# Kernel optimization log

Hardware: AMD Instinct MI355X
Metric: run time of the kernel (lower is better)

Reference implementation:

```python
import jax, jax.numpy as jnp
import numpy as np

B, D, N, M = 32, 512, 1024, 1024

def setup_inputs() -> dict:
    key = jax.random.key(0)
    k1, k2 = jax.random.split(key)
    embedding_1 = jax.random.normal(k1, (B, D, N), dtype=jnp.float32)
    embedding_2 = jax.random.normal(k2, (B, D, M), dtype=jnp.float32)
    return {"embedding_1": embedding_1, "embedding_2": embedding_2}

def reference(embedding_1, embedding_2):
    # att[b, n, m] = sum_d e1[b, d, n] * e2[b, d, m]   (bmm of e1^T with e2)
    att = jnp.einsum('bdn,bdm->bnm', embedding_1, embedding_2)
    # double max-pool: max over m then over n -> global max of score matrix
    s = jnp.max(att, axis=(-1, -2))  # [B]
    return s[:, None]  # [B, 1]
```

## Files before the change

### kernel.cpp

```cpp
#include <hip/hip_runtime.h>
#include <hip/hip_bf16.h>

#define B_ 32
#define D_ 512
#define N_ 1024
#define M_ 1024
#define BT 256
#define BK 64
#define NIT 16

typedef __attribute__((ext_vector_type(8))) short bf16x8;
typedef __attribute__((ext_vector_type(4))) short s16x4;
typedef __attribute__((ext_vector_type(4))) float f32x4;
typedef __attribute__((ext_vector_type(4))) int   i32x4;
typedef unsigned short ushort_t;

__device__ __forceinline__ unsigned map_f(float f) {
    unsigned b = __float_as_uint(f);
    return (b & 0x80000000u) ? ~b : (b | 0x80000000u);
}

struct __align__(16) GSmem {
    ushort_t As[2][BT * BK];
    ushort_t Bs[2][BT * BK];
    float red[8];
};

__device__ __forceinline__ void load_tile(const float* __restrict__ p, int k0,
                                          int krb, int gr, float4* fl) {
    #pragma unroll
    for (int it = 0; it < 4; ++it) {
        const float* q = p + (size_t)(k0 + krb + it) * N_ + gr * 8;
        fl[2 * it]     = *reinterpret_cast<const float4*>(q);
        fl[2 * it + 1] = *reinterpret_cast<const float4*>(q + 4);
    }
}

__device__ __forceinline__ void flush_tile(char* lds, int krb, int gr, const float4* fl) {
    #pragma unroll
    for (int it = 0; it < 4; ++it) {
        const int k = krb + it;
        const float4& f0 = fl[2 * it];
        const float4& f1 = fl[2 * it + 1];
        __hip_bfloat162 h0 = __float22bfloat162_rn(make_float2(f0.x, f0.y));
        __hip_bfloat162 h1 = __float22bfloat162_rn(make_float2(f0.z, f0.w));
        __hip_bfloat162 h2 = __float22bfloat162_rn(make_float2(f1.x, f1.y));
        __hip_bfloat162 h3 = __float22bfloat162_rn(make_float2(f1.z, f1.w));
        i32x4 v = { *reinterpret_cast<const int*>(&h0), *reinterpret_cast<const int*>(&h1),
                    *reinterpret_cast<const int*>(&h2), *reinterpret_cast<const int*>(&h3) };
        *reinterpret_cast<i32x4*>(lds + k * 512 + 16 * (gr ^ (2 * (k & 3)))) = v;
    }
}

__global__ __launch_bounds__(512, 2)
void fused_gemm_max_kernel(const float* __restrict__ e1, const float* __restrict__ e2,
                           float* __restrict__ out) {
    __shared__ GSmem sm;
    const int wg  = blockIdx.x;
    const int swz = (wg & 7) * 32 + (wg >> 3);
    const int b    = swz >> 3;
    const int pair = swz & 7;
    const int tn  = (pair >> 1) * BT;
    const int tc0 = (pair & 1) * 512;

    const int t    = threadIdx.x;
    const int lane = t & 63;
    const int wave = t >> 6;
    const int wrow = (wave >> 2) * 128;
    const int wcol = (wave & 3) * 64;

    const int krb = (t >> 5) * 4;
    const int gr  = t & 31;

    const int c = lane & 15, g = lane >> 4;
    const int r = c >> 2, d = (c >> 1) & 1, h = c & 1;

    unsigned tbA[8], tbB[4];
    #pragma unroll
    for (int m = 0; m < 8; ++m)
        tbA[m] = (unsigned)((8 * g + r) * 512
               + 16 * ((((wrow >> 3) + 2 * m + d) ^ (2 * r))) + 8 * h);
    #pragma unroll
    for (int n = 0; n < 4; ++n)
        tbB[n] = (unsigned)(65536 + (8 * g + r) * 512
               + 16 * ((((wcol >> 3) + 2 * n + d) ^ (2 * r))) + 8 * h);
    const unsigned ldsbase = (unsigned)(uintptr_t)&sm.As[0][0];

    const float* Ap  = e1 + (size_t)b * D_ * N_ + tn;
    const float* Bp0 = e2 + (size_t)b * D_ * M_ + tc0;
    const float* Bp1 = Bp0 + BT;

    f32x4 acc[8][4] = {};
    float4 fl[8];
    float tmax = -3.4e38f;

    load_tile(Ap, 0, krb, gr, fl);
    flush_tile((char*)sm.As[0], krb, gr, fl);
    load_tile(Bp0, 0, krb, gr, fl);
    flush_tile((char*)sm.Bs[0], krb, gr, fl);
    load_tile(Ap, BK, krb, gr, fl);
    asm volatile("s_waitcnt lgkmcnt(0)" ::: "memory");
    __builtin_amdgcn_s_barrier();

    int cur = 0;
    #pragma unroll 1
    for (int it = 0; it < NIT; ++it) {
        const unsigned off = ldsbase + (unsigned)cur * 32768u;
        const bool has_next = (it < NIT - 1);

        #pragma unroll
        for (int kk = 0; kk < 2; ++kk) {
            s16x4 alo[8], ahi[8], blo[4], bhi[4];
            #pragma unroll
            for (int m = 0; m < 8; ++m) {
                asm volatile("ds_read_b64_tr_b16 %0, %1 offset:%2"
                             : "=v"(alo[m]) : "v"(tbA[m] + off), "n"(kk * 16384));
                asm volatile("ds_read_b64_tr_b16 %0, %1 offset:%2"
                             : "=v"(ahi[m]) : "v"(tbA[m] + off), "n"(kk * 16384 + 2048));
            }
            #pragma unroll
            for (int n = 0; n < 4; ++n) {
                asm volatile("ds_read_b64_tr_b16 %0, %1 offset:%2"
                             : "=v"(blo[n]) : "v"(tbB[n] + off), "n"(kk * 16384));
                asm volatile("ds_read_b64_tr_b16 %0, %1 offset:%2"
                             : "=v"(bhi[n]) : "v"(tbB[n] + off), "n"(kk * 16384 + 2048));
            }
            asm volatile("s_waitcnt lgkmcnt(0)" ::: "memory");
            __builtin_amdgcn_sched_barrier(0);
            bf16x8 af[8], bf[4];
            #pragma unroll
            for (int m = 0; m < 8; ++m)
                af[m] = __builtin_shufflevector(alo[m], ahi[m], 0, 1, 2, 3, 4, 5, 6, 7);
            #pragma unroll
            for (int n = 0; n < 4; ++n)
                bf[n] = __builtin_shufflevector(blo[n], bhi[n], 0, 1, 2, 3, 4, 5, 6, 7);
            __builtin_amdgcn_s_setprio(1);
            #pragma unroll
            for (int m = 0; m < 8; ++m)
                #pragma unroll
                for (int n = 0; n < 4; ++n)
                    acc[m][n] = __builtin_amdgcn_mfma_f32_16x16x32_bf16(
                        af[m], bf[n], acc[m][n], 0, 0, 0);
            __builtin_amdgcn_s_setprio(0);

            if (kk == 0 && has_next) {
                flush_tile((char*)sm.As[cur ^ 1], krb, gr, fl);
                const float* bp = (it + 1 < 8) ? Bp0 : Bp1;
                load_tile(bp, ((it + 1) & 7) * BK, krb, gr, fl);
            }
        }

        if (it == 7) {
            #pragma unroll
            for (int m = 0; m < 8; ++m)
                #pragma unroll
                for (int n = 0; n < 4; ++n) {
                    #pragma unroll
                    for (int i = 0; i < 4; ++i)
                        tmax = fmaxf(tmax, acc[m][n][i]);
                    acc[m][n] = f32x4{0.f, 0.f, 0.f, 0.f};
                }
        }

        if (has_next) {
            flush_tile((char*)sm.Bs[cur ^ 1], krb, gr, fl);
            if (it < NIT - 2)
                load_tile(Ap, ((it + 2) & 7) * BK, krb, gr, fl);
        }
        asm volatile("s_waitcnt lgkmcnt(0)" ::: "memory");
        __builtin_amdgcn_s_barrier();
        cur ^= 1;
    }

    #pragma unroll
    for (int m = 0; m < 8; ++m)
        #pragma unroll
        for (int n = 0; n < 4; ++n)
            #pragma unroll
            for (int i = 0; i < 4; ++i)
                tmax = fmaxf(tmax, acc[m][n][i]);
    #pragma unroll
    for (int off2 = 32; off2; off2 >>= 1)
        tmax = fmaxf(tmax, __shfl_xor(tmax, off2));
    if (lane == 0) sm.red[wave] = tmax;
    __syncthreads();
    if (t == 0) {
        float m8 = sm.red[0];
        #pragma unroll
        for (int w = 1; w < 8; ++w) m8 = fmaxf(m8, sm.red[w]);
        atomicMax(reinterpret_cast<unsigned*>(out) + b, map_f(m8));
    }
}

__global__ void finalize_kernel(float* out) {
    const int i = threadIdx.x;
    unsigned u = reinterpret_cast<unsigned*>(out)[i];
    out[i] = __uint_as_float((u & 0x80000000u) ? (u ^ 0x80000000u) : ~u);
}

extern "C" void kernel_launch(void* const* d_in, const int* in_sizes, int n_in,
                              void* d_out, int out_size, void* d_ws, size_t ws_size,
                              hipStream_t stream) {
    const float* e1 = (const float*)d_in[0];
    const float* e2 = (const float*)d_in[1];
    float* out = (float*)d_out;

    (void)hipMemsetAsync(d_out, 0, B_ * sizeof(float), stream);

    fused_gemm_max_kernel<<<dim3(256), 512, 0, stream>>>(e1, e2, out);
    finalize_kernel<<<1, B_, 0, stream>>>(out);
}
```

Measured before the change: 50.99 us.

## Store tiles K-contiguous in LDS and read fragments with plain vector loads

Changes the LDS staging layout from row-per-k with transposing reads to column-per-n with 8 consecutive k values packed per 16-byte chunk. The conversion now happens in registers during the flush, so the MFMA fragments can be loaded with ordinary 128-bit ds_read instead of paired ds_read_b64_tr_b16 instructions. Global loads now fetch one float4 across 8 different k rows per thread, which makes per-wave coalescing narrower. The explicit waitcnt, sched_barrier and setprio hints are also dropped, leaving scheduling to the compiler.

```diff
diff --git a/kernel.cpp b/kernel.cpp
--- a/kernel.cpp
+++ b/kernel.cpp
@@ -10,7 +10,6 @@
 #define NIT 16
 
 typedef __attribute__((ext_vector_type(8))) short bf16x8;
-typedef __attribute__((ext_vector_type(4))) short s16x4;
 typedef __attribute__((ext_vector_type(4))) float f32x4;
 typedef __attribute__((ext_vector_type(4))) int   i32x4;
 typedef unsigned short ushort_t;
@@ -27,28 +26,32 @@
 };
 
 __device__ __forceinline__ void load_tile(const float* __restrict__ p, int k0,
-                                          int krb, int gr, float4* fl) {
+                                          int q, int jg, float4* fl) {
+    const float* base = p + (size_t)(k0 + q * 8) * N_ + jg * 4;
     #pragma unroll
-    for (int it = 0; it < 4; ++it) {
-        const float* q = p + (size_t)(k0 + krb + it) * N_ + gr * 8;
-        fl[2 * it]     = *reinterpret_cast<const float4*>(q);
-        fl[2 * it + 1] = *reinterpret_cast<const float4*>(q + 4);
-    }
+    for (int dd = 0; dd < 8; ++dd)
+        fl[dd] = *reinterpret_cast<const float4*>(base + (size_t)dd * N_);
 }
 
-__device__ __forceinline__ void flush_tile(char* lds, int krb, int gr, const float4* fl) {
+__device__ __forceinline__ void flush_tile(char* lds, int q, int jg, const float4* fl) {
     #pragma unroll
-    for (int it = 0; it < 4; ++it) {
-        const int k = krb + it;
-        const float4& f0 = fl[2 * it];
-        const float4& f1 = fl[2 * it + 1];
-        __hip_bfloat162 h0 = __float22bfloat162_rn(make_float2(f0.x, f0.y));
-        __hip_bfloat162 h1 = __float22bfloat162_rn(make_float2(f0.z, f0.w));
-        __hip_bfloat162 h2 = __float22bfloat162_rn(make_float2(f1.x, f1.y));
-        __hip_bfloat162 h3 = __float22bfloat162_rn(make_float2(f1.z, f1.w));
+    for (int ji = 0; ji < 4; ++ji) {
+        const int j = jg * 4 + ji;
+        __hip_bfloat162 h0 = __float22bfloat162_rn(
+            make_float2(reinterpret_cast<const float*>(&fl[0])[ji],
+                        reinterpret_cast<const float*>(&fl[1])[ji]));
+        __hip_bfloat162 h1 = __float22bfloat162_rn(
+            make_float2(reinterpret_cast<const float*>(&fl[2])[ji],
+                        reinterpret_cast<const float*>(&fl[3])[ji]));
+        __hip_bfloat162 h2 = __float22bfloat162_rn(
+            make_float2(reinterpret_cast<const float*>(&fl[4])[ji],
+                        reinterpret_cast<const float*>(&fl[5])[ji]));
+        __hip_bfloat162 h3 = __float22bfloat162_rn(
+            make_float2(reinterpret_cast<const float*>(&fl[6])[ji],
+                        reinterpret_cast<const float*>(&fl[7])[ji]));
         i32x4 v = { *reinterpret_cast<const int*>(&h0), *reinterpret_cast<const int*>(&h1),
                     *reinterpret_cast<const int*>(&h2), *reinterpret_cast<const int*>(&h3) };
-        *reinterpret_cast<i32x4*>(lds + k * 512 + 16 * (gr ^ (2 * (k & 3)))) = v;
+        *reinterpret_cast<i32x4*>(lds + j * 128 + 16 * (q ^ (j & 7))) = v;
     }
 }
 
@@ -69,22 +72,23 @@
     const int wrow = (wave >> 2) * 128;
     const int wcol = (wave & 3) * 64;
 
-    const int krb = (t >> 5) * 4;
-    const int gr  = t & 31;
+    const int q  = t & 7;
+    const int jg = t >> 3;
 
-    const int c = lane & 15, g = lane >> 4;
-    const int r = c >> 2, d = (c >> 1) & 1, h = c & 1;
-
-    unsigned tbA[8], tbB[4];
+    const int l15 = lane & 15;
+    const int l4  = lane >> 4;
+    unsigned uA[8], uB[4];
     #pragma unroll
-    for (int m = 0; m < 8; ++m)
-        tbA[m] = (unsigned)((8 * g + r) * 512
-               + 16 * ((((wrow >> 3) + 2 * m + d) ^ (2 * r))) + 8 * h);
+    for (int m = 0; m < 8; ++m) {
+        const int j = wrow + m * 16 + l15;
+        uA[m] = (unsigned)(j * 128 + 16 * (l4 ^ (j & 7)));
+    }
     #pragma unroll
-    for (int n = 0; n < 4; ++n)
-        tbB[n] = (unsigned)(65536 + (8 * g + r) * 512
-               + 16 * ((((wcol >> 3) + 2 * n + d) ^ (2 * r))) + 8 * h);
-    const unsigned ldsbase = (unsigned)(uintptr_t)&sm.As[0][0];
+    for (int n = 0; n < 4; ++n) {
+        const int j = wcol + n * 16 + l15;
+        uB[n] = (unsigned)(65536 + j * 128 + 16 * (l4 ^ (j & 7)));
+    }
+    const char* ldsb = (const char*)&sm.As[0][0];
 
     const float* Ap  = e1 + (size_t)b * D_ * N_ + tn;
     const float* Bp0 = e2 + (size_t)b * D_ * M_ + tc0;
@@ -94,59 +98,41 @@
     float4 fl[8];
     float tmax = -3.4e38f;
 
-    load_tile(Ap, 0, krb, gr, fl);
-    flush_tile((char*)sm.As[0], krb, gr, fl);
-    load_tile(Bp0, 0, krb, gr, fl);
-    flush_tile((char*)sm.Bs[0], krb, gr, fl);
-    load_tile(Ap, BK, krb, gr, fl);
+    load_tile(Ap, 0, q, jg, fl);
+    flush_tile((char*)sm.As[0], q, jg, fl);
+    load_tile(Bp0, 0, q, jg, fl);
+    flush_tile((char*)sm.Bs[0], q, jg, fl);
+    load_tile(Ap, BK, q, jg, fl);
     asm volatile("s_waitcnt lgkmcnt(0)" ::: "memory");
     __builtin_amdgcn_s_barrier();
 
     int cur = 0;
     #pragma unroll 1
     for (int it = 0; it < NIT; ++it) {
-        const unsigned off = ldsbase + (unsigned)cur * 32768u;
+        const unsigned off = (unsigned)cur * 32768u;
         const bool has_next = (it < NIT - 1);
 
         #pragma unroll
         for (int kk = 0; kk < 2; ++kk) {
-            s16x4 alo[8], ahi[8], blo[4], bhi[4];
-            #pragma unroll
-            for (int m = 0; m < 8; ++m) {
-                asm volatile("ds_read_b64_tr_b16 %0, %1 offset:%2"
-                             : "=v"(alo[m]) : "v"(tbA[m] + off), "n"(kk * 16384));
-                asm volatile("ds_read_b64_tr_b16 %0, %1 offset:%2"
-                             : "=v"(ahi[m]) : "v"(tbA[m] + off), "n"(kk * 16384 + 2048));
-            }
-            #pragma unroll
-            for (int n = 0; n < 4; ++n) {
-                asm volatile("ds_read_b64_tr_b16 %0, %1 offset:%2"
-                             : "=v"(blo[n]) : "v"(tbB[n] + off), "n"(kk * 16384));
-                asm volatile("ds_read_b64_tr_b16 %0, %1 offset:%2"
-                             : "=v"(bhi[n]) : "v"(tbB[n] + off), "n"(kk * 16384 + 2048));
-            }
-            asm volatile("s_waitcnt lgkmcnt(0)" ::: "memory");
-            __builtin_amdgcn_sched_barrier(0);
+            const unsigned kx = (unsigned)(kk << 6);
             bf16x8 af[8], bf[4];
             #pragma unroll
             for (int m = 0; m < 8; ++m)
-                af[m] = __builtin_shufflevector(alo[m], ahi[m], 0, 1, 2, 3, 4, 5, 6, 7);
+                af[m] = *reinterpret_cast<const bf16x8*>(ldsb + off + (uA[m] ^ kx));
             #pragma unroll
             for (int n = 0; n < 4; ++n)
-                bf[n] = __builtin_shufflevector(blo[n], bhi[n], 0, 1, 2, 3, 4, 5, 6, 7);
-            __builtin_amdgcn_s_setprio(1);
+                bf[n] = *reinterpret_cast<const bf16x8*>(ldsb + off + (uB[n] ^ kx));
             #pragma unroll
             for (int m = 0; m < 8; ++m)
                 #pragma unroll
                 for (int n = 0; n < 4; ++n)
                     acc[m][n] = __builtin_amdgcn_mfma_f32_16x16x32_bf16(
                         af[m], bf[n], acc[m][n], 0, 0, 0);
-            __builtin_amdgcn_s_setprio(0);
 
             if (kk == 0 && has_next) {
-                flush_tile((char*)sm.As[cur ^ 1], krb, gr, fl);
+                flush_tile((char*)sm.As[cur ^ 1], q, jg, fl);
                 const float* bp = (it + 1 < 8) ? Bp0 : Bp1;
-                load_tile(bp, ((it + 1) & 7) * BK, krb, gr, fl);
+                load_tile(bp, ((it + 1) & 7) * BK, q, jg, fl);
             }
         }
 
@@ -163,9 +149,9 @@
         }
 
         if (has_next) {
-            flush_tile((char*)sm.Bs[cur ^ 1], krb, gr, fl);
+            flush_tile((char*)sm.Bs[cur ^ 1], q, jg, fl);
             if (it < NIT - 2)
-                load_tile(Ap, ((it + 2) & 7) * BK, krb, gr, fl);
+                load_tile(Ap, ((it + 2) & 7) * BK, q, jg, fl);
         }
         asm volatile("s_waitcnt lgkmcnt(0)" ::: "memory");
         __builtin_amdgcn_s_barrier();
```

New measurement: 71.70 us. 1.41x slower.
